# Kernel tuning notes

Measured on AMD Instinct MI355X. Metric: run time of the kernel, lower is better.

Reference implementation:

```python
import jax, jax.numpy as jnp
import numpy as np

T_SYN = 201
SYN_BASIS_NO = 3


def setup_inputs() -> dict:
    key = jax.random.key(0)
    ks = jax.random.split(key, 5)
    T_data, n_e, n_i, sub_no, B = 100000, 500, 200, 20, SYN_BASIS_NO
    S_e = jax.random.uniform(ks[0], (T_data, n_e), jnp.float32)
    S_i = jax.random.uniform(ks[1], (T_data, n_i), jnp.float32)
    C_syn_e = jax.random.uniform(ks[2], (sub_no, n_e), jnp.float32)
    C_syn_i = jax.random.uniform(ks[3], (sub_no, n_i), jnp.float32)
    # init values from the torch module
    K_syn = jnp.concatenate([jnp.full((sub_no, B, 1), 0.02, jnp.float32),
                             jnp.full((sub_no, B, 1), -0.02, jnp.float32)], axis=-1)
    tau_syn = jnp.tile(jnp.arange(1.6, 1.6 + B, dtype=jnp.float32).reshape(-1, 1), (1, 2))
    delta_syn = 2.0 * jax.random.uniform(ks[4], (sub_no, 2), jnp.float32)
    return dict(S_e=S_e, S_i=S_i, C_syn_e=C_syn_e, C_syn_i=C_syn_i,
                K_syn=K_syn, tau_syn=tau_syn, delta_syn=delta_syn)


def _kernels(K_syn, tau_syn, delta_syn):
    # Vectorized alpha-function kernel bank: [sub_no, 2(e/i), T_syn]
    t = jnp.arange(T_SYN, dtype=jnp.float32)                     # [T]
    ts = t[None, None, :] - delta_syn[:, :, None]                # [S,2,T]
    ts = jnp.where(ts < 0.0, 0.0, ts)                            # clamp like t[t<0]=0
    tau = jnp.exp(tau_syn)                                       # [B,2]
    tt = ts[:, None, :, :] / tau[None, :, :, None]               # [S,B,2,T]
    basis = tt * jnp.exp(-tt)                                    # alpha functions
    return jnp.einsum('sbct,sbc->sct', basis, K_syn)             # [S,2,T]


def _causal_conv(x, kern):
    # x: [T_data, S]; kern: [S, T_syn]; out[t,s] = sum_k kern[s,k] * x[t-k,s]
    S = x.shape[1]
    lhs = x.T[None]                          # [1,S,T_data]
    rhs = kern[:, ::-1][:, None, :]          # flip -> lax correlation == causal conv
    out = jax.lax.conv_general_dilated(lhs, rhs, (1,), [(T_SYN - 1, 0)],
                                       feature_group_count=S,
                                       dimension_numbers=('NCH', 'OIH', 'NCH'))
    return out[0].T                          # [T_data, S]


def reference(S_e, S_i, C_syn_e, C_syn_i, K_syn, tau_syn, delta_syn):
    kern = _kernels(K_syn, tau_syn, delta_syn)   # [S,2,T_syn]
    in_e = S_e @ C_syn_e.T                       # [T_data, sub_no]
    in_i = S_i @ C_syn_i.T                       # [T_data, sub_no]
    return _causal_conv(in_e, kern[:, 0]) + _causal_conv(in_i, kern[:, 1])
```

## Files before the change

kernel.cpp:

```cpp
#include <hip/hip_runtime.h>
#include <hip/hip_bf16.h>

#define TDATA 100000
#define NE 500
#define NI 200
#define SUB 20
#define NB 3
#define TSYN 201

#define SROW 100552
#define HROW 216
#define STEPS_E 32
#define STEPS_I 13
#define FULL_E 31
#define FULL_I 12
#define GEMM_BLKS 782

#define OFF_HP  0
#define OFF_BE  8640
#define OFF_BI  (OFF_BE + 8192)
#define OFF_INT (OFF_BI + 3328)

typedef __bf16 bf16x8 __attribute__((ext_vector_type(8)));
typedef float  f32x16 __attribute__((ext_vector_type(16)));

__global__ __launch_bounds__(256) void setup_kernel(
    const float* __restrict__ C_e, const float* __restrict__ C_i,
    const float* __restrict__ K_syn, const float* __restrict__ tau_syn,
    const float* __restrict__ delta_syn, float* __restrict__ ws)
{
    int idx = blockIdx.x * 256 + threadIdx.x;
    if (idx < 8640) {
        int c = idx / (SUB * HROW);
        int rem = idx - c * (SUB * HROW);
        int s = rem / HROW;
        int k = (rem - s * HROW) - 8;
        float v = 0.f;
        if (k >= 0 && k < TSYN) {
            float ts = (float)k - delta_syn[s * 2 + c];
            ts = ts < 0.f ? 0.f : ts;
            #pragma unroll
            for (int b = 0; b < NB; b++) {
                float tt = ts / expf(tau_syn[b * 2 + c]);
                v += K_syn[(s * NB + b) * 2 + c] * tt * expf(-tt);
            }
        }
        ws[OFF_HP + idx] = v;
    } else if (idx < 30720) {
        int j = idx - 8640;
        const int PERROW = 552;
        int row = j / PERROW;
        int e = j - row * PERROW;
        int off = (e < 200) ? e : (200 + TDATA + (e - 200));
        ws[OFF_INT + (long)row * SROW + off] = 0.f;
    } else if (idx < 47104) {
        int j = idx - 30720;
        int step = j >> 9;
        int lane = (j >> 3) & 63;
        int jj = j & 7;
        int k = step * 16 + ((lane >> 5) << 3) + jj;
        int s = lane & 31;
        float v = (s < SUB && k < NE) ? C_e[s * NE + k] : 0.f;
        ((__hip_bfloat16*)(ws + OFF_BE))[j] = (__hip_bfloat16)v;
    } else {
        int j = idx - 47104;
        int step = j >> 9;
        int lane = (j >> 3) & 63;
        int jj = j & 7;
        int k = step * 16 + ((lane >> 5) << 3) + jj;
        int s = lane & 31;
        float v = (s < SUB && k < NI) ? C_i[s * NI + k] : 0.f;
        ((__hip_bfloat16*)(ws + OFF_BI))[j] = (__hip_bfloat16)v;
    }
}

template<int K, int FULL>
__device__ __forceinline__ void gemm_body(
    const float* __restrict__ S, const float* __restrict__ wsA,
    float* __restrict__ inT, long row0, int lane)
{
    const int n = lane & 31, h = lane >> 5;
    long row = row0 + n; if (row >= TDATA) row = TDATA - 1;
    const float* rp = S + row * (long)K + h * 8;
    const bf16x8* afr = (const bf16x8*)wsA;
    f32x16 acc = {};

    #pragma unroll 4
    for (int u = 0; u < FULL; u++) {
        float4 lo = *(const float4*)(rp + 16 * u);
        float4 hi = *(const float4*)(rp + 16 * u + 4);
        bf16x8 b;
        b[0] = (__bf16)lo.x; b[1] = (__bf16)lo.y; b[2] = (__bf16)lo.z; b[3] = (__bf16)lo.w;
        b[4] = (__bf16)hi.x; b[5] = (__bf16)hi.y; b[6] = (__bf16)hi.z; b[7] = (__bf16)hi.w;
        bf16x8 a = afr[u * 64 + lane];
        acc = __builtin_amdgcn_mfma_f32_32x32x16_bf16(a, b, acc, 0, 0, 0);
    }
    {
        int kb = FULL * 16 + h * 8;
        float4 lo = make_float4(0.f, 0.f, 0.f, 0.f);
        float4 hi = make_float4(0.f, 0.f, 0.f, 0.f);
        if (kb + 8 <= K) {
            lo = *(const float4*)(rp + 16 * FULL);
            hi = *(const float4*)(rp + 16 * FULL + 4);
        } else if (kb + 4 <= K) {
            lo = *(const float4*)(rp + 16 * FULL);
        }
        bf16x8 b;
        b[0] = (__bf16)lo.x; b[1] = (__bf16)lo.y; b[2] = (__bf16)lo.z; b[3] = (__bf16)lo.w;
        b[4] = (__bf16)hi.x; b[5] = (__bf16)hi.y; b[6] = (__bf16)hi.z; b[7] = (__bf16)hi.w;
        bf16x8 a = afr[FULL * 64 + lane];
        acc = __builtin_amdgcn_mfma_f32_32x32x16_bf16(a, b, acc, 0, 0, 0);
    }

    long t = row0 + n;
    #pragma unroll
    for (int r = 0; r < 16; r++) {
        int m = (r & 3) + 8 * (r >> 2) + 4 * h;
        if (m < SUB && t < TDATA)
            inT[(long)m * SROW + 200 + t] = acc[r];
    }
}

__global__ __launch_bounds__(256) void gemm_kernel(
    const float* __restrict__ Se, const float* __restrict__ Si,
    float* __restrict__ ws)
{
    int lane = threadIdx.x & 63, wave = threadIdx.x >> 6;
    if (blockIdx.x < GEMM_BLKS) {
        long row0 = (long)blockIdx.x * 128 + wave * 32;
        gemm_body<NE, FULL_E>(Se, ws + OFF_BE, ws + OFF_INT, row0, lane);
    } else {
        long row0 = (long)(blockIdx.x - GEMM_BLKS) * 128 + wave * 32;
        gemm_body<NI, FULL_I>(Si, ws + OFF_BI,
                              ws + OFF_INT + (long)SUB * SROW, row0, lane);
    }
}

#define SW(i) ((i) + ((i) >> 5))

__global__ __launch_bounds__(256) void conv_kernel(
    const float* __restrict__ ws, float* __restrict__ out)
{
    __shared__ __align__(16) float W[2][2336];
    __shared__ __align__(16) float HT[2][208];
    const int tid = threadIdx.x;
    const int s = blockIdx.y;
    const long t0 = (long)blockIdx.x * 2048;

    for (int i = tid; i < 1128; i += 256) {
        int c = i >= 564;
        int i4 = i - c * 564;
        float4 v = *(const float4*)(ws + OFF_INT + (long)(c * SUB + s) * SROW
                                    + t0 - 8 + 4 * i4);
        int b = 4 * i4;
        int p = SW(b);
        W[c][p] = v.x; W[c][p + 1] = v.y; W[c][p + 2] = v.z; W[c][p + 3] = v.w;
    }
    if (tid < 104) {
        int c = tid >= 52;
        int j4 = (tid - c * 52) * 4;
        *(float4*)&HT[c][j4] =
            *(const float4*)(ws + OFF_HP + (c * SUB + s) * HROW + 8 + j4);
    }
    __syncthreads();

    float acc[8];
    #pragma unroll
    for (int r = 0; r < 8; r++) acc[r] = 0.f;

    #pragma unroll
    for (int c = 0; c < 2; c++) {
        #pragma unroll 2
        for (int g = 0; g < 26; g++) {
            int k0 = g << 3;
            int xb = (tid << 3) + 200 - k0;
            float x[16];
            #pragma unroll
            for (int q = 0; q < 16; q++) x[q] = W[c][SW(xb + q)];
            float h[8];
            *(float4*)&h[0] = *(const float4*)&HT[c][k0];
            *(float4*)&h[4] = *(const float4*)&HT[c][k0 + 4];
            #pragma unroll
            for (int j = 0; j < 8; j++)
                #pragma unroll
                for (int r = 0; r < 8; r++)
                    acc[r] += h[j] * x[8 + r - j];
        }
    }

    #pragma unroll
    for (int r = 0; r < 8; r++) {
        long t = t0 + 8 * tid + r;
        if (t < TDATA) out[t * SUB + s] = acc[r];
    }
}

extern "C" void kernel_launch(void* const* d_in, const int* in_sizes, int n_in,
                              void* d_out, int out_size, void* d_ws, size_t ws_size,
                              hipStream_t stream)
{
    const float* S_e     = (const float*)d_in[0];
    const float* S_i     = (const float*)d_in[1];
    const float* C_e     = (const float*)d_in[2];
    const float* C_i     = (const float*)d_in[3];
    const float* K_syn   = (const float*)d_in[4];
    const float* tau_syn = (const float*)d_in[5];
    const float* delta   = (const float*)d_in[6];
    float* out = (float*)d_out;
    float* ws  = (float*)d_ws;

    hipLaunchKernelGGL(setup_kernel, dim3(210), dim3(256), 0, stream,
                       C_e, C_i, K_syn, tau_syn, delta, ws);
    hipLaunchKernelGGL(gemm_kernel, dim3(2 * GEMM_BLKS), dim3(256), 0, stream,
                       S_e, S_i, ws);
    hipLaunchKernelGGL(conv_kernel, dim3(49, SUB), dim3(256), 0, stream,
                       ws, out);
}
```

Before: 409.5 us.

## Stage GEMM rows in LDS with split-K across waves; reuse conv input registers

Each GEMM block now covers 32 rows. It loads them coalesced into LDS, splits the K dimension across the four waves with A fragments preloaded into registers, and reduces the partial MFMA accumulators through LDS. This replaces strided per-lane global loads with coalesced ones. The conv inner loop now keeps a sliding register window, loading only 8 new LDS values per step instead of 16, which halves LDS reads. The cost is a large LDS footprint (about 64KB) that limits GEMM occupancy, plus extra synchronisation for the reduction.

```diff
diff --git a/kernel.cpp b/kernel.cpp
--- a/kernel.cpp
+++ b/kernel.cpp
@@ -12,9 +12,7 @@
 #define HROW 216
 #define STEPS_E 32
 #define STEPS_I 13
-#define FULL_E 31
-#define FULL_I 12
-#define GEMM_BLKS 782
+#define GEMM_BLKS 3125
 
 #define OFF_HP  0
 #define OFF_BE  8640
@@ -74,65 +72,92 @@
     }
 }
 
-template<int K, int FULL>
-__device__ __forceinline__ void gemm_body(
-    const float* __restrict__ S, const float* __restrict__ wsA,
-    float* __restrict__ inT, long row0, int lane)
-{
-    const int n = lane & 31, h = lane >> 5;
-    long row = row0 + n; if (row >= TDATA) row = TDATA - 1;
-    const float* rp = S + row * (long)K + h * 8;
-    const bf16x8* afr = (const bf16x8*)wsA;
-    f32x16 acc = {};
-
-    #pragma unroll 4
-    for (int u = 0; u < FULL; u++) {
-        float4 lo = *(const float4*)(rp + 16 * u);
-        float4 hi = *(const float4*)(rp + 16 * u + 4);
-        bf16x8 b;
-        b[0] = (__bf16)lo.x; b[1] = (__bf16)lo.y; b[2] = (__bf16)lo.z; b[3] = (__bf16)lo.w;
-        b[4] = (__bf16)hi.x; b[5] = (__bf16)hi.y; b[6] = (__bf16)hi.z; b[7] = (__bf16)hi.w;
-        bf16x8 a = afr[u * 64 + lane];
-        acc = __builtin_amdgcn_mfma_f32_32x32x16_bf16(a, b, acc, 0, 0, 0);
-    }
-    {
-        int kb = FULL * 16 + h * 8;
-        float4 lo = make_float4(0.f, 0.f, 0.f, 0.f);
-        float4 hi = make_float4(0.f, 0.f, 0.f, 0.f);
-        if (kb + 8 <= K) {
-            lo = *(const float4*)(rp + 16 * FULL);
-            hi = *(const float4*)(rp + 16 * FULL + 4);
-        } else if (kb + 4 <= K) {
-            lo = *(const float4*)(rp + 16 * FULL);
-        }
-        bf16x8 b;
-        b[0] = (__bf16)lo.x; b[1] = (__bf16)lo.y; b[2] = (__bf16)lo.z; b[3] = (__bf16)lo.w;
-        b[4] = (__bf16)hi.x; b[5] = (__bf16)hi.y; b[6] = (__bf16)hi.z; b[7] = (__bf16)hi.w;
-        bf16x8 a = afr[FULL * 64 + lane];
-        acc = __builtin_amdgcn_mfma_f32_32x32x16_bf16(a, b, acc, 0, 0, 0);
-    }
-
-    long t = row0 + n;
-    #pragma unroll
-    for (int r = 0; r < 16; r++) {
-        int m = (r & 3) + 8 * (r >> 2) + 4 * h;
-        if (m < SUB && t < TDATA)
-            inT[(long)m * SROW + 200 + t] = acc[r];
-    }
-}
-
 __global__ __launch_bounds__(256) void gemm_kernel(
     const float* __restrict__ Se, const float* __restrict__ Si,
     float* __restrict__ ws)
 {
-    int lane = threadIdx.x & 63, wave = threadIdx.x >> 6;
-    if (blockIdx.x < GEMM_BLKS) {
-        long row0 = (long)blockIdx.x * 128 + wave * 32;
-        gemm_body<NE, FULL_E>(Se, ws + OFF_BE, ws + OFF_INT, row0, lane);
-    } else {
-        long row0 = (long)(blockIdx.x - GEMM_BLKS) * 128 + wave * 32;
-        gemm_body<NI, FULL_I>(Si, ws + OFF_BI,
-                              ws + OFF_INT + (long)SUB * SROW, row0, lane);
+    __shared__ float lds[16016];
+    const int tid  = threadIdx.x;
+    const int lane = tid & 63, w = tid >> 6;
+    const bool isE = blockIdx.x < GEMM_BLKS;
+    const int blk  = isE ? blockIdx.x : blockIdx.x - GEMM_BLKS;
+    const float* S = isE ? Se : Si;
+    const int KROW = isE ? NE : NI;
+    const int NV4  = isE ? 4000 : 1600;
+    const int ZTAIL = isE ? 16000 : 6400;
+    const float* afr_base = ws + (isE ? OFF_BE : OFF_BI);
+    float* inT = ws + OFF_INT + (isE ? 0 : (long)SUB * SROW);
+    const long row0 = (long)blk * 32;
+
+    int u0, u1;
+    if (isE) { u0 = 8 * w; u1 = u0 + 8; }
+    else     { u0 = (w == 0) ? 0 : (w == 1) ? 4 : (w == 2) ? 7 : 10;
+               u1 = (w == 0) ? 4 : (w == 1) ? 7 : (w == 2) ? 10 : 13; }
+
+    const bf16x8* afr = (const bf16x8*)afr_base;
+    bf16x8 af[8];
+    #pragma unroll
+    for (int p = 0; p < 8; p++) {
+        int u = u0 + p;
+        if (u < u1) af[p] = afr[u * 64 + lane];
+    }
+
+    const float4* g4 = (const float4*)(S + row0 * (long)KROW);
+    #pragma unroll 1
+    for (int j0 = 0; j0 < NV4; j0 += 1024) {
+        float4 v[4];
+        #pragma unroll
+        for (int p = 0; p < 4; p++) {
+            int j = j0 + p * 256 + tid;
+            if (j < NV4) v[p] = g4[j];
+        }
+        #pragma unroll
+        for (int p = 0; p < 4; p++) {
+            int j = j0 + p * 256 + tid;
+            if (j < NV4) *(float4*)&lds[4 * j] = v[p];
+        }
+    }
+    if (tid < 4) *(float4*)&lds[ZTAIL + 4 * tid] = make_float4(0.f, 0.f, 0.f, 0.f);
+    __syncthreads();
+
+    const int n = lane & 31, h = lane >> 5;
+    const int bbase = n * KROW + 8 * h;
+    f32x16 acc = {};
+    #pragma unroll
+    for (int p = 0; p < 8; p++) {
+        int u = u0 + p;
+        if (u < u1) {
+            float4 lo = *(const float4*)&lds[bbase + 16 * u];
+            float4 hi = *(const float4*)&lds[bbase + 16 * u + 4];
+            bf16x8 b;
+            b[0] = (__bf16)lo.x; b[1] = (__bf16)lo.y;
+            b[2] = (__bf16)lo.z; b[3] = (__bf16)lo.w;
+            b[4] = (__bf16)hi.x; b[5] = (__bf16)hi.y;
+            b[6] = (__bf16)hi.z; b[7] = (__bf16)hi.w;
+            acc = __builtin_amdgcn_mfma_f32_32x32x16_bf16(af[p], b, acc, 0, 0, 0);
+        }
+    }
+
+    __syncthreads();
+    if (w > 0) {
+        float* rb = &lds[(w - 1) * 1024];
+        #pragma unroll
+        for (int q = 0; q < 16; q++) rb[q * 64 + lane] = acc[q];
+    }
+    __syncthreads();
+    if (w == 0) {
+        #pragma unroll
+        for (int ww = 0; ww < 3; ww++) {
+            const float* rb = &lds[ww * 1024];
+            #pragma unroll
+            for (int q = 0; q < 16; q++) acc[q] += rb[q * 64 + lane];
+        }
+        long t = row0 + n;
+        #pragma unroll
+        for (int r = 0; r < 16; r++) {
+            int m = (r & 3) + 8 * (r >> 2) + 4 * h;
+            if (m < SUB) inT[(long)m * SROW + 200 + t] = acc[r];
+        }
     }
 }
 
@@ -152,8 +177,7 @@
         int i4 = i - c * 564;
         float4 v = *(const float4*)(ws + OFF_INT + (long)(c * SUB + s) * SROW
                                     + t0 - 8 + 4 * i4);
-        int b = 4 * i4;
-        int p = SW(b);
+        int p = SW(4 * i4);
         W[c][p] = v.x; W[c][p + 1] = v.y; W[c][p + 2] = v.z; W[c][p + 3] = v.w;
     }
     if (tid < 104) {
@@ -170,21 +194,30 @@
 
     #pragma unroll
     for (int c = 0; c < 2; c++) {
+        const int xb0 = (tid << 3) + 200;
+        float x[16];
+        #pragma unroll
+        for (int q = 0; q < 16; q++) x[q] = W[c][SW(xb0 + q)];
         #pragma unroll 2
         for (int g = 0; g < 26; g++) {
-            int k0 = g << 3;
-            int xb = (tid << 3) + 200 - k0;
-            float x[16];
-            #pragma unroll
-            for (int q = 0; q < 16; q++) x[q] = W[c][SW(xb + q)];
             float h[8];
-            *(float4*)&h[0] = *(const float4*)&HT[c][k0];
-            *(float4*)&h[4] = *(const float4*)&HT[c][k0 + 4];
+            *(float4*)&h[0] = *(const float4*)&HT[c][g * 8];
+            *(float4*)&h[4] = *(const float4*)&HT[c][g * 8 + 4];
             #pragma unroll
             for (int j = 0; j < 8; j++)
                 #pragma unroll
                 for (int r = 0; r < 8; r++)
                     acc[r] += h[j] * x[8 + r - j];
+            if (g < 25) {
+                float nx[8];
+                #pragma unroll
+                for (int q = 0; q < 8; q++)
+                    nx[q] = W[c][SW(xb0 - 8 * (g + 1) + q)];
+                #pragma unroll
+                for (int q = 0; q < 8; q++) x[8 + q] = x[q];
+                #pragma unroll
+                for (int q = 0; q < 8; q++) x[q] = nx[q];
+            }
         }
     }
 
```

Result: slower. 453.8 us (+10.8%).
